# Kernel optimization log

Measured on AMD Instinct MI355X. Metric: run time of the kernel, lower is better.

Reference implementation:

```python
import jax, jax.numpy as jnp
import numpy as np

P = 16          # patch size (patch_height == patch_width)
DIM = 768       # feature dim
K = 9           # number of anchor boxes (arange(0, 9) in source)
# anchor_boxes = [(h_ratio, w_ratio) for h in (2,4,8) for w in (2,4,8)]
BOX_H = jnp.array([2., 2., 2., 4., 4., 4., 8., 8., 8.], dtype=jnp.float32)
BOX_W = jnp.array([2., 4., 8., 2., 4., 8., 2., 4., 8.], dtype=jnp.float32)


def setup_inputs() -> dict:
    key = jax.random.key(0)
    k0, k1, k2, k3 = jax.random.split(key, 4)
    b, c, h, w = 32, 3, 512, 512
    img = jax.random.normal(k0, (b, c, h, w), dtype=jnp.float32)
    # patch-embed stand-in for feature_extraction_ViT: (c*P*P) -> DIM
    w_patch = jax.random.normal(k1, (c * P * P, DIM), dtype=jnp.float32) * 0.02
    w_reg = jax.random.normal(k2, (DIM, 4 * K), dtype=jnp.float32) * 0.02
    b_reg = jnp.zeros((4 * K,), dtype=jnp.float32)
    w_obj = jax.random.normal(k3, (DIM, K), dtype=jnp.float32) * 0.02
    b_obj = jnp.zeros((K,), dtype=jnp.float32)
    return {"img": img, "w_patch": w_patch, "w_reg": w_reg, "b_reg": b_reg,
            "w_obj": w_obj, "b_obj": b_obj}


def reference(img, w_patch, w_reg, b_reg, w_obj, b_obj):
    b, c, h, w = img.shape
    fh, fw = h // P, w // P
    # --- feature_extraction_ViT (patch embedding) -> feature map [b, fh, fw, DIM]
    patches = img.reshape(b, c, fh, P, fw, P).transpose(0, 2, 4, 1, 3, 5)
    patches = patches.reshape(b, fh, fw, c * P * P)
    feat = patches @ w_patch                                  # [b, fh, fw, DIM]
    # --- RPN: regs [b, fh, fw, K, 4], objectness [b, fh, fw, K, 1]
    regs = (feat @ w_reg + b_reg).reshape(b, fh, fw, K, 4)    # separate_anchor_boxes, s=4
    is_object = jax.nn.sigmoid(feat @ w_obj + b_obj)[..., None]
    # --- anchor-box coordinate decoding (memory-bound broadcast pipeline)
    wgrid = jnp.arange(0, w, P, dtype=jnp.float32)            # step = patch_width
    hgrid = jnp.arange(0, h, P, dtype=jnp.float32)            # step = patch_height
    width_coords = wgrid[None, None, :, None, None] + regs[..., 0:1]
    height_coords = hgrid[None, :, None, None, None] + regs[..., 1:2]
    width_abs = width_coords + BOX_W[None, None, None, :, None] * regs[..., 2:3]
    height_abs = height_coords + BOX_H[None, None, None, :, None] * regs[..., 3:4]
    batch_idx = jnp.broadcast_to(
        jnp.arange(b, dtype=jnp.float32)[:, None, None, None, None], (b, fh, fw, K, 1))
    k_idx = jnp.broadcast_to(
        jnp.arange(K, dtype=jnp.float32)[None, None, None, :, None], (b, fh, fw, K, 1))
    merged = jnp.concatenate(
        [width_coords, height_coords, width_abs, height_abs, batch_idx, is_object, k_idx],
        axis=-1)                                              # [b, fh, fw, K, 7]
    tensor_reshaped = merged.reshape(-1, 7)                   # (b h w k) x
    return tensor_reshaped
```

## Files before the change

kernel.cpp:

```cpp
#include <hip/hip_runtime.h>
#include <hip/hip_bf16.h>

typedef __attribute__((ext_vector_type(8))) short bf16x8;
typedef __attribute__((ext_vector_type(4))) float f32x4;

__device__ __forceinline__ unsigned short f2bf(float f) {
    unsigned int u = __float_as_uint(f);
    u = (u + 0x7FFFu + ((u >> 16) & 1u)) >> 16;
    return (unsigned short)u;
}

__device__ __forceinline__ unsigned int pkbf(float x, float y) {
    __hip_bfloat162 h = __float22bfloat162_rn(float2{x, y});
    unsigned int u;
    __builtin_memcpy(&u, &h, 4);
    return u;
}

__global__ __launch_bounds__(256) void btrans(
        const float* __restrict__ wreg, const float* __restrict__ wobj,
        float* __restrict__ Bt) {
    const int idx = blockIdx.x * 256 + threadIdx.x;
    const int n = idx / 768, d = idx - n * 768;
    float v = 0.f;
    if (n < 36)      v = wreg[(size_t)d * 36 + n];
    else if (n < 45) v = wobj[(size_t)d * 9 + (n - 36)];
    Bt[idx] = v;
}

__global__ __launch_bounds__(256) void wcomb_partial2(
        const float* __restrict__ wp, const float* __restrict__ Bt,
        float* __restrict__ part) {
    __shared__ float Al[16][132];
    __shared__ float Bl[48][132];
    const int t  = threadIdx.x;
    const int kb = blockIdx.x * 16;
    const int dc = blockIdx.y;
    const int d0 = dc * 128;

    #pragma unroll
    for (int i = 0; i < 2; ++i) {
        int e = i * 256 + t;
        int row = e >> 5, v = e & 31;
        *(f32x4*)&Al[row][v * 4] =
            *(const f32x4*)&wp[(size_t)(kb + row) * 768 + d0 + v * 4];
    }
    #pragma unroll
    for (int i = 0; i < 6; ++i) {
        int e = i * 256 + t;
        int row = e >> 5, v = e & 31;
        *(f32x4*)&Bl[row][v * 4] =
            *(const f32x4*)&Bt[(size_t)row * 768 + d0 + v * 4];
    }
    __syncthreads();

    const int k  = t >> 4;
    const int n0 = (t & 15) * 3;
    float acc[3] = {0.f, 0.f, 0.f};
    #pragma unroll 8
    for (int ds = 0; ds < 32; ++ds) {
        f32x4 a = *(const f32x4*)&Al[k][ds * 4];
        #pragma unroll
        for (int j = 0; j < 3; ++j) {
            f32x4 b = *(const f32x4*)&Bl[n0 + j][ds * 4];
            acc[j] += a.x * b.x + a.y * b.y + a.z * b.z + a.w * b.w;
        }
    }
    #pragma unroll
    for (int j = 0; j < 3; ++j)
        part[((size_t)dc * 768 + kb + k) * 48 + n0 + j] = acc[j];
}

__global__ __launch_bounds__(256) void wcomb_reduce2(
        const float* __restrict__ part, unsigned short* __restrict__ wct) {
    const int idx = blockIdx.x * 256 + threadIdx.x;
    const int n = idx / 768, k = idx - n * 768;
    float s = 0.f;
    if (n < 45) {
        #pragma unroll
        for (int dc = 0; dc < 6; ++dc) s += part[((size_t)dc * 768 + k) * 48 + n];
    }
    wct[idx] = f2bf(s);
}

__global__ __launch_bounds__(256) void detector_main(
        const float* __restrict__ img, const unsigned short* __restrict__ wct,
        const float* __restrict__ breg, const float* __restrict__ bobj,
        float* __restrict__ out) {
    __shared__ float Co[4][16][49];

    const int t    = threadIdx.x;
    const int lane = t & 63;
    const int wid  = t >> 6;
    const int cl   = lane & 15;
    const int q    = lane >> 4;
    const int tg   = blockIdx.x;
    const int fj0  = (tg & 1) * 16;
    const int fi   = (tg >> 1) & 31;
    const int b    = tg >> 6;
    const int k0   = wid * 6;

    const float* abase = img + (size_t)b * 786432
        + (size_t)(fi * 16 + (q >> 1)) * 512 + (fj0 + cl) * 16 + (q & 1) * 8;
    const unsigned short* bbase = wct + cl * 768 + q * 8;

    #define AOFF(kk) ((size_t)((kk) >> 3) * 262144 + (size_t)((kk) & 7) * 1024)

    f32x4 acc0 = {0.f,0.f,0.f,0.f}, acc1 = acc0, acc2 = acc0;

    f32x4 a0lo = *(const f32x4*)(abase + AOFF(k0));
    f32x4 a0hi = *(const f32x4*)(abase + AOFF(k0) + 4);
    f32x4 a1lo = *(const f32x4*)(abase + AOFF(k0 + 1));
    f32x4 a1hi = *(const f32x4*)(abase + AOFF(k0 + 1) + 4);
    bf16x8 b0x = *(const bf16x8*)(bbase + (size_t)k0 * 32);
    bf16x8 b0y = *(const bf16x8*)(bbase + (size_t)k0 * 32 + 12288);
    bf16x8 b0z = *(const bf16x8*)(bbase + (size_t)k0 * 32 + 24576);

    #pragma unroll
    for (int i = 0; i < 6; ++i) {
        f32x4 a2lo, a2hi;
        if (i < 4) {
            a2lo = *(const f32x4*)(abase + AOFF(k0 + i + 2));
            a2hi = *(const f32x4*)(abase + AOFF(k0 + i + 2) + 4);
        } else { a2lo = a1lo; a2hi = a1hi; }
        bf16x8 b1x, b1y, b1z;
        if (i < 5) {
            b1x = *(const bf16x8*)(bbase + (size_t)(k0 + i + 1) * 32);
            b1y = *(const bf16x8*)(bbase + (size_t)(k0 + i + 1) * 32 + 12288);
            b1z = *(const bf16x8*)(bbase + (size_t)(k0 + i + 1) * 32 + 24576);
        } else { b1x = b0x; b1y = b0y; b1z = b0z; }

        union { bf16x8 v; unsigned int u[4]; } af;
        af.u[0] = pkbf(a0lo.x, a0lo.y);
        af.u[1] = pkbf(a0lo.z, a0lo.w);
        af.u[2] = pkbf(a0hi.x, a0hi.y);
        af.u[3] = pkbf(a0hi.z, a0hi.w);
        acc0 = __builtin_amdgcn_mfma_f32_16x16x32_bf16(af.v, b0x, acc0, 0, 0, 0);
        acc1 = __builtin_amdgcn_mfma_f32_16x16x32_bf16(af.v, b0y, acc1, 0, 0, 0);
        acc2 = __builtin_amdgcn_mfma_f32_16x16x32_bf16(af.v, b0z, acc2, 0, 0, 0);

        a0lo = a1lo; a0hi = a1hi; a1lo = a2lo; a1hi = a2hi;
        b0x = b1x; b0y = b1y; b0z = b1z;
    }
    #undef AOFF

    #pragma unroll
    for (int r = 0; r < 4; ++r) {
        Co[wid][q * 4 + r][ 0 + cl] = acc0[r];
        Co[wid][q * 4 + r][16 + cl] = acc1[r];
        Co[wid][q * 4 + r][32 + cl] = acc2[r];
    }
    __syncthreads();

    for (int rr = t; rr < 144; rr += 256) {
        int cell = rr / 9, k = rr - cell * 9;
        int dfj  = fj0 + cell;
        float v0 = Co[0][cell][4*k+0] + Co[1][cell][4*k+0]
                 + Co[2][cell][4*k+0] + Co[3][cell][4*k+0] + breg[4*k+0];
        float v1 = Co[0][cell][4*k+1] + Co[1][cell][4*k+1]
                 + Co[2][cell][4*k+1] + Co[3][cell][4*k+1] + breg[4*k+1];
        float v2 = Co[0][cell][4*k+2] + Co[1][cell][4*k+2]
                 + Co[2][cell][4*k+2] + Co[3][cell][4*k+2] + breg[4*k+2];
        float v3 = Co[0][cell][4*k+3] + Co[1][cell][4*k+3]
                 + Co[2][cell][4*k+3] + Co[3][cell][4*k+3] + breg[4*k+3];
        float lg = Co[0][cell][36+k]  + Co[1][cell][36+k]
                 + Co[2][cell][36+k]  + Co[3][cell][36+k]  + bobj[k];
        float obj = 1.f / (1.f + __expf(-lg));
        float wc = (float)(dfj * 16) + v0;
        float hc = (float)(fi * 16) + v1;
        float wa = wc + (float)(2 << (k % 3)) * v2;
        float ha = hc + (float)(2 << (k / 3)) * v3;
        float* o = out + (size_t)(((b * 32 + fi) * 32 + dfj) * 9 + k) * 7;
        o[0] = wc; o[1] = hc; o[2] = wa; o[3] = ha;
        o[4] = (float)b; o[5] = obj; o[6] = (float)k;
    }
}

extern "C" void kernel_launch(void* const* d_in, const int* in_sizes, int n_in,
                              void* d_out, int out_size, void* d_ws, size_t ws_size,
                              hipStream_t stream) {
    const float* img  = (const float*)d_in[0];
    const float* wp   = (const float*)d_in[1];
    const float* wreg = (const float*)d_in[2];
    const float* breg = (const float*)d_in[3];
    const float* wobj = (const float*)d_in[4];
    const float* bobj = (const float*)d_in[5];
    float* out = (float*)d_out;

    unsigned short* wct = (unsigned short*)d_ws;
    float* Bt   = (float*)((char*)d_ws + 73728);
    float* part = (float*)((char*)d_ws + 73728 + 147456);

    btrans<<<144, 256, 0, stream>>>(wreg, wobj, Bt);
    wcomb_partial2<<<dim3(48, 6), 256, 0, stream>>>(wp, Bt, part);
    wcomb_reduce2<<<144, 256, 0, stream>>>(part, wct);
    detector_main<<<2048, 256, 0, stream>>>(img, wct, breg, bobj, out);
}
```

Baseline: 174.3 us.

## Fuse weight-combine transpose, partial GEMM and reduction into one kernel

Replaces the three weight-preprocessing kernels (transpose, split-D partial products, reduction) with a single kernel. Each block of 512 threads computes 8 rows of the combined w_patch·[w_reg|w_obj] product and loads the head weights straight into shared memory, with no intermediate transpose buffer. This removes two kernel launches and the workspace round trips. In exchange, only 96 blocks run, each looping over 768 dimensions, and shared-memory use per block is larger.

```diff
diff --git a/kernel.cpp b/kernel.cpp
--- a/kernel.cpp
+++ b/kernel.cpp
@@ -17,70 +17,55 @@
     return u;
 }
 
-__global__ __launch_bounds__(256) void btrans(
-        const float* __restrict__ wreg, const float* __restrict__ wobj,
-        float* __restrict__ Bt) {
-    const int idx = blockIdx.x * 256 + threadIdx.x;
-    const int n = idx / 768, d = idx - n * 768;
-    float v = 0.f;
-    if (n < 36)      v = wreg[(size_t)d * 36 + n];
-    else if (n < 45) v = wobj[(size_t)d * 9 + (n - 36)];
-    Bt[idx] = v;
-}
+__global__ __launch_bounds__(512) void wcomb_fused(
+        const float* __restrict__ wp, const float* __restrict__ wreg,
+        const float* __restrict__ wobj, unsigned short* __restrict__ wct) {
+    __shared__ float Al[8 * 384];
+    __shared__ float Bw[384 * 52];
 
-__global__ __launch_bounds__(256) void wcomb_partial2(
-        const float* __restrict__ wp, const float* __restrict__ Bt,
-        float* __restrict__ part) {
-    __shared__ float Al[16][132];
-    __shared__ float Bl[48][132];
-    const int t  = threadIdx.x;
-    const int kb = blockIdx.x * 16;
-    const int dc = blockIdx.y;
-    const int d0 = dc * 128;
+    const int t    = threadIdx.x;
+    const int w    = t >> 6;
+    const int lane = t & 63;
+    const int kg   = blockIdx.x * 8 + w;
+
+    float acc = 0.f;
 
     #pragma unroll
-    for (int i = 0; i < 2; ++i) {
-        int e = i * 256 + t;
-        int row = e >> 5, v = e & 31;
-        *(f32x4*)&Al[row][v * 4] =
-            *(const f32x4*)&wp[(size_t)(kb + row) * 768 + d0 + v * 4];
-    }
-    #pragma unroll
-    for (int i = 0; i < 6; ++i) {
-        int e = i * 256 + t;
-        int row = e >> 5, v = e & 31;
-        *(f32x4*)&Bl[row][v * 4] =
-            *(const f32x4*)&Bt[(size_t)row * 768 + d0 + v * 4];
-    }
-    __syncthreads();
+    for (int ch = 0; ch < 2; ++ch) {
+        const int d0 = ch * 384;
+        if (ch) __syncthreads();
 
-    const int k  = t >> 4;
-    const int n0 = (t & 15) * 3;
-    float acc[3] = {0.f, 0.f, 0.f};
-    #pragma unroll 8
-    for (int ds = 0; ds < 32; ++ds) {
-        f32x4 a = *(const f32x4*)&Al[k][ds * 4];
-        #pragma unroll
-        for (int j = 0; j < 3; ++j) {
-            f32x4 b = *(const f32x4*)&Bl[n0 + j][ds * 4];
-            acc[j] += a.x * b.x + a.y * b.y + a.z * b.z + a.w * b.w;
+        for (int e = t; e < 768; e += 512) {
+            int r = e / 96, j = e - r * 96;
+            *(f32x4*)&Al[r * 384 + j * 4] =
+                *(const f32x4*)&wp[(size_t)(blockIdx.x * 8 + r) * 768 + d0 + j * 4];
+        }
+        for (int e = t; e < 3456; e += 512) {
+            int r = e / 9, j = e - r * 9;
+            *(f32x4*)&Bw[r * 52 + j * 4] =
+                *(const f32x4*)&wreg[(size_t)(d0 + r) * 36 + j * 4];
+        }
+        for (int e = t; e < 3456; e += 512) {
+            int r = e / 9, c = e - r * 9;
+            Bw[r * 52 + 36 + c] = wobj[(size_t)(d0 + r) * 9 + c];
+        }
+        __syncthreads();
+
+        if (lane < 45) {
+            const float* alr = &Al[w * 384];
+            #pragma unroll 8
+            for (int j = 0; j < 96; ++j) {
+                f32x4 a = *(const f32x4*)&alr[j * 4];
+                acc += a.x * Bw[(j * 4 + 0) * 52 + lane]
+                     + a.y * Bw[(j * 4 + 1) * 52 + lane]
+                     + a.z * Bw[(j * 4 + 2) * 52 + lane]
+                     + a.w * Bw[(j * 4 + 3) * 52 + lane];
+            }
         }
     }
-    #pragma unroll
-    for (int j = 0; j < 3; ++j)
-        part[((size_t)dc * 768 + kb + k) * 48 + n0 + j] = acc[j];
-}
 
-__global__ __launch_bounds__(256) void wcomb_reduce2(
-        const float* __restrict__ part, unsigned short* __restrict__ wct) {
-    const int idx = blockIdx.x * 256 + threadIdx.x;
-    const int n = idx / 768, k = idx - n * 768;
-    float s = 0.f;
-    if (n < 45) {
-        #pragma unroll
-        for (int dc = 0; dc < 6; ++dc) s += part[((size_t)dc * 768 + k) * 48 + n];
-    }
-    wct[idx] = f2bf(s);
+    if (lane < 45)      wct[(size_t)lane * 768 + kg] = f2bf(acc);
+    else if (lane < 48) wct[(size_t)lane * 768 + kg] = 0;
 }
 
 __global__ __launch_bounds__(256) void detector_main(
@@ -188,11 +173,7 @@
     float* out = (float*)d_out;
 
     unsigned short* wct = (unsigned short*)d_ws;
-    float* Bt   = (float*)((char*)d_ws + 73728);
-    float* part = (float*)((char*)d_ws + 73728 + 147456);
 
-    btrans<<<144, 256, 0, stream>>>(wreg, wobj, Bt);
-    wcomb_partial2<<<dim3(48, 6), 256, 0, stream>>>(wp, Bt, part);
-    wcomb_reduce2<<<144, 256, 0, stream>>>(part, wct);
+    wcomb_fused<<<96, 512, 0, stream>>>(wp, wreg, wobj, wct);
     detector_main<<<2048, 256, 0, stream>>>(img, wct, breg, bobj, out);
 }
```

New measurement: 188.6 us. 1.08x slower.
